# Kernel tuning notes

Measured on AMD Instinct MI355X. Metric: run time of the kernel, lower is better.

## Reference

```python
import jax, jax.numpy as jnp
import numpy as np

HEAD_DIM = 6
WS = 8  # window size
GROUPS = 4
EPS = 1e-5


def conv3x3(x, w, b):
    y = jax.lax.conv_general_dilated(x, w, (1, 1), [(1, 1), (1, 1)],
                                     dimension_numbers=('NCHW', 'OIHW', 'NCHW'))
    return y + b[None, :, None, None]


def conv1x1(x, w, b):
    # w: (O, C, 1, 1) pointwise conv == channel matmul
    return jnp.einsum('bchw,oc->bohw', x, w[:, :, 0, 0]) + b[None, :, None, None]


def group_norm(x, gamma, beta):
    B, C, H, W = x.shape
    xg = x.reshape(B, GROUPS, C // GROUPS, H, W)
    mu = xg.mean(axis=(2, 3, 4), keepdims=True)
    var = xg.var(axis=(2, 3, 4), keepdims=True)
    xg = (xg - mu) * jax.lax.rsqrt(var + EPS)
    return xg.reshape(B, C, H, W) * gamma[None, :, None, None] + beta[None, :, None, None]


def window_attention(x, qkv_w, qkv_b, proj_w, proj_b):
    # Per-window channel attention (attn is head_dim x head_dim, softmax over last dim).
    B, C, H, W = x.shape
    heads = C // HEAD_DIM
    scale = HEAD_DIM ** -0.5
    Hn, Wn = H // WS, W // WS
    L = WS * WS
    qkv = conv1x1(x, qkv_w, qkv_b)                       # (B, 3C, H, W); 1x1 conv commutes with windowing
    qkv = qkv.reshape(B, 3, heads, HEAD_DIM, Hn, WS, Wn, WS)
    qkv = qkv.transpose(1, 0, 4, 6, 2, 3, 5, 7).reshape(3, B, Hn, Wn, heads, HEAD_DIM, L)
    q, k, v = qkv[0], qkv[1], qkv[2]
    attn = jnp.einsum('bijhdl,bijhel->bijhde', q, k) * scale  # (B,Hn,Wn,heads,hd,hd)
    attn = jax.nn.softmax(attn, axis=-1)
    out = jnp.einsum('bijhde,bijhel->bijhdl', attn, v)
    out = out.reshape(B, Hn, Wn, heads, HEAD_DIM, WS, WS)
    out = out.transpose(0, 3, 4, 1, 5, 2, 6).reshape(B, C, H, W)
    return conv1x1(out, proj_w, proj_b)


def shifted_window_attention(x, qkv_w, qkv_b, proj_w, proj_b):
    B, C, H, W = x.shape
    pad_h = (WS - H % WS) % WS
    pad_w = (WS - W % WS) % WS
    if pad_h or pad_w:
        x = jnp.pad(x, ((0, 0), (0, 0), (0, pad_h), (0, pad_w)), mode='reflect')
    s = WS // 2
    x_sh = jnp.roll(x, shift=(-s, -s), axis=(2, 3))
    x1 = window_attention(x, qkv_w, qkv_b, proj_w, proj_b)
    x2 = window_attention(x_sh, qkv_w, qkv_b, proj_w, proj_b)
    x2 = jnp.roll(x2, shift=(s, s), axis=(2, 3))
    x = (x1 + x2) * 0.5
    return x[:, :, :H, :W]


def setup_inputs() -> dict:
    key = jax.random.key(0)
    ks = jax.random.split(key, 12)
    B, Cin, Cout, T, H, W = 16, 96, 96, 256, 128, 128
    std = 0.05
    return {
        'x': jax.random.normal(ks[0], (B, Cin, H, W), jnp.float32),
        't_emb': jax.random.normal(ks[1], (B, T), jnp.float32),
        'w1': jax.random.normal(ks[2], (Cout, Cin, 3, 3), jnp.float32) * std,
        'b1': jnp.zeros((Cout,), jnp.float32),
        'g1': jnp.ones((Cout,), jnp.float32),
        'be1': jnp.zeros((Cout,), jnp.float32),
        'wt': jax.random.normal(ks[3], (2 * Cout, T), jnp.float32) * std,
        'bt': jnp.zeros((2 * Cout,), jnp.float32),
        'qkv_w': jax.random.normal(ks[4], (3 * Cout, Cout, 1, 1), jnp.float32) * std,
        'qkv_b': jnp.zeros((3 * Cout,), jnp.float32),
        'proj_w': jax.random.normal(ks[5], (Cout, Cout, 1, 1), jnp.float32) * std,
        'proj_b': jnp.zeros((Cout,), jnp.float32),
        'ga': jnp.ones((Cout,), jnp.float32),
        'ba': jnp.zeros((Cout,), jnp.float32),
        'w2': jax.random.normal(ks[6], (Cout, Cout, 3, 3), jnp.float32) * std,
        'b2': jnp.zeros((Cout,), jnp.float32),
        'g2': jnp.ones((Cout,), jnp.float32),
        'be2': jnp.zeros((Cout,), jnp.float32),
    }


def reference(x, t_emb, w1, b1, g1, be1, wt, bt, qkv_w, qkv_b, proj_w, proj_b,
              ga, ba, w2, b2, g2, be2):
    C = w1.shape[0]
    # layer1: conv3x3 -> GN(4) -> SiLU
    h = jax.nn.silu(group_norm(conv3x3(x, w1, b1), g1, be1))
    # time FiLM
    t = jax.nn.silu(t_emb @ wt.T + bt)             # (B, 2C)
    shift, bias = t[:, :C], t[:, C:]
    h = h * (1.0 + shift[:, :, None, None]) + bias[:, :, None, None]
    residual = h
    h = group_norm(h, ga, ba)
    h = shifted_window_attention(h, qkv_w, qkv_b, proj_w, proj_b)
    h = residual + h
    # layer2: conv3x3 -> GN(4) -> SiLU
    h = jax.nn.silu(group_norm(conv3x3(h, w2, b2), g2, be2))
    return h
```

## Files before the change

kernel.cpp:

```cpp
#include <hip/hip_runtime.h>

#define B_   16
#define C_   96
#define H_   128
#define W_   128
#define HW_  16384
#define CPG_ 24
#define NPG_ 393216.0f
#define TDIM_ 256
#define PLANE_ ((size_t)B_ * C_ * HW_)

typedef unsigned short ushort_t;
typedef __bf16 bf16x8 __attribute__((ext_vector_type(8)));
typedef float  f32x4  __attribute__((ext_vector_type(4)));
typedef unsigned short u16x8 __attribute__((ext_vector_type(8)));
typedef unsigned short u16x4 __attribute__((ext_vector_type(4)));

#define ICP 104

__device__ __forceinline__ float silu_f(float x) { return x / (1.f + __expf(-x)); }
__device__ __forceinline__ float bf2f(ushort_t u) {
    union { float f; unsigned int i; } x; x.i = ((unsigned int)u) << 16; return x.f;
}
__device__ __forceinline__ ushort_t f2bf(float f) {
    __bf16 h = (__bf16)f; return *(ushort_t*)&h;
}

__global__ void temb_kernel(const float* __restrict__ t_emb,
                            const float* __restrict__ wt,
                            const float* __restrict__ bt,
                            float* __restrict__ tvec) {
    int idx = blockIdx.x * 256 + threadIdx.x;
    if (idx >= B_ * 192) return;
    int b = idx / 192, o = idx - b * 192;
    float a = bt[o];
    const float* te = t_emb + b * TDIM_;
    const float* wr = wt + o * TDIM_;
    for (int k = 0; k < TDIM_; ++k) a += te[k] * wr[k];
    tvec[idx] = silu_f(a);
}

__global__ void castbf_kernel(const float* __restrict__ src,
                              ushort_t* __restrict__ dst, int n4) {
    int i = blockIdx.x * 256 + threadIdx.x;
    if (i >= n4) return;
    float4 v = ((const float4*)src)[i];
    ushort4 u = { f2bf(v.x), f2bf(v.y), f2bf(v.z), f2bf(v.w) };
    ((ushort4*)dst)[i] = u;
}

__global__ void castw_kernel(const float* __restrict__ w1,
                             const float* __restrict__ w2,
                             ushort_t* __restrict__ wbf1,
                             ushort_t* __restrict__ wbf2) {
    int i = blockIdx.x * 256 + threadIdx.x;
    int ic = i % 96;
    int t  = i / 96;
    int oc = t % 96;
    int kk = t / 96;
    int src = (oc * 96 + ic) * 9 + kk;
    wbf1[i] = f2bf(w1[src]);
    wbf2[i] = f2bf(w2[src]);
}

__global__ __launch_bounds__(256, 2)
void conv3x3_mfma_kernel(const ushort_t* __restrict__ xbf,
                         const ushort_t* __restrict__ wbf,
                         const float* __restrict__ bias,
                         float* __restrict__ out,
                         float* __restrict__ stats) {
    __shared__ __align__(16) ushort_t ti[4 * 66 * ICP];
    __shared__ __align__(16) ushort_t wc[96 * ICP];
    __shared__ float red[4][96][2];

    const int b   = blockIdx.z;
    const int y0  = blockIdx.y * 2;
    const int x0  = blockIdx.x * 64;
    const int tid = threadIdx.x;
    const int wv   = tid >> 6;
    const int lane = tid & 63;
    const int l15  = lane & 15;
    const int quad = lane >> 4;

#pragma unroll
    for (int it = 0; it < 12; ++it) {
        int idx = it * 256 + tid;
        int ic = idx % 96;
        int t2 = idx / 96;
        int xc = t2 & 7;
        int r  = t2 >> 3;
        int gy = y0 - 1 + r;
        u16x8 v = {};
        if (gy >= 0 && gy < H_)
            v = *(const u16x8*)&xbf[((b * 96 + ic) * H_ + gy) * W_ + x0 + xc * 8];
        ushort_t* dst = &ti[(r * 66 + xc * 8 + 1) * ICP + ic];
#pragma unroll
        for (int j = 0; j < 8; ++j) dst[j * ICP] = v[j];
    }
    {
        int idx = tid;
#pragma unroll
        for (int it = 0; it < 3; ++it, idx += 256) {
            int ic = idx % 96;
            int t2 = idx / 96;
            int r = t2 >> 1, side = t2 & 1;
            int xi = side ? 65 : 0;
            int gx = x0 - 1 + xi;
            int gy = y0 - 1 + r;
            ushort_t vv = 0;
            if (gy >= 0 && gy < H_ && gx >= 0 && gx < W_)
                vv = xbf[((b * 96 + ic) * H_ + gy) * W_ + gx];
            ti[(r * 66 + xi) * ICP + ic] = vv;
        }
    }

    int wsrc[5], wdst[5];
#pragma unroll
    for (int i = 0; i < 5; ++i) {
        int idx = tid + i * 256;
        int icb = idx % 12;
        int oc  = idx / 12;
        wsrc[i] = oc * 96 + icb * 8;
        wdst[i] = oc * ICP + icb * 8;
    }
    u16x8 wreg[5];
#pragma unroll
    for (int i = 0; i < 4; ++i) wreg[i] = *(const u16x8*)&wbf[wsrc[i]];
    if (tid < 128) wreg[4] = *(const u16x8*)&wbf[wsrc[4]];

    f32x4 acc[2][6];
#pragma unroll
    for (int m = 0; m < 2; ++m)
#pragma unroll
        for (int nt = 0; nt < 6; ++nt)
            acc[m][nt] = (f32x4){0.f, 0.f, 0.f, 0.f};

    for (int kk = 0; kk < 9; ++kk) {
        const int ky = kk / 3, kx = kk - ky * 3;
        __syncthreads();
#pragma unroll
        for (int i = 0; i < 4; ++i) *(u16x8*)&wc[wdst[i]] = wreg[i];
        if (tid < 128) *(u16x8*)&wc[wdst[4]] = wreg[4];
        __syncthreads();
        if (kk < 8) {
            const ushort_t* wsk = wbf + (kk + 1) * 9216;
#pragma unroll
            for (int i = 0; i < 4; ++i) wreg[i] = *(const u16x8*)&wsk[wsrc[i]];
            if (tid < 128) wreg[4] = *(const u16x8*)&wsk[wsrc[4]];
        }
#pragma unroll 1
        for (int ck = 0; ck < 3; ++ck) {
            const int kbase = ck * 32 + quad * 8;
            bf16x8 a0 = *(const bf16x8*)&ti[((0 + ky) * 66 + (wv * 16 + l15 + kx)) * ICP + kbase];
            bf16x8 a1 = *(const bf16x8*)&ti[((1 + ky) * 66 + (wv * 16 + l15 + kx)) * ICP + kbase];
#pragma unroll
            for (int nt = 0; nt < 6; ++nt) {
                bf16x8 bv = *(const bf16x8*)&wc[(nt * 16 + l15) * ICP + kbase];
                acc[0][nt] = __builtin_amdgcn_mfma_f32_16x16x32_bf16(a0, bv, acc[0][nt], 0, 0, 0);
                acc[1][nt] = __builtin_amdgcn_mfma_f32_16x16x32_bf16(a1, bv, acc[1][nt], 0, 0, 0);
            }
        }
    }

    float lsum[6], lsq[6];
#pragma unroll
    for (int nt = 0; nt < 6; ++nt) { lsum[nt] = 0.f; lsq[nt] = 0.f; }

#pragma unroll
    for (int m = 0; m < 2; ++m) {
        const int gy = y0 + m;
        const int gx = x0 + wv * 16 + quad * 4;
#pragma unroll
        for (int nt = 0; nt < 6; ++nt) {
            const int oc = nt * 16 + l15;
            const float bz = bias[oc];
            float v0 = acc[m][nt][0] + bz;
            float v1 = acc[m][nt][1] + bz;
            float v2 = acc[m][nt][2] + bz;
            float v3 = acc[m][nt][3] + bz;
            float4 vv = make_float4(v0, v1, v2, v3);
            *(float4*)&out[((b * 96 + oc) * H_ + gy) * W_ + gx] = vv;
            lsum[nt] += v0 + v1 + v2 + v3;
            lsq[nt]  += v0 * v0 + v1 * v1 + v2 * v2 + v3 * v3;
        }
    }
#pragma unroll
    for (int nt = 0; nt < 6; ++nt) {
        float s = lsum[nt], q = lsq[nt];
        s += __shfl_down(s, 32, 64);
        s += __shfl_down(s, 16, 64);
        q += __shfl_down(q, 32, 64);
        q += __shfl_down(q, 16, 64);
        if (lane < 16) {
            red[wv][nt * 16 + lane][0] = s;
            red[wv][nt * 16 + lane][1] = q;
        }
    }
    __syncthreads();
    if (tid < 8) {
        const int g = tid >> 1, which = tid & 1;
        float v = 0.f;
        for (int oc = g * CPG_; oc < g * CPG_ + CPG_; ++oc)
            for (int w2 = 0; w2 < 4; ++w2) v += red[w2][oc][which];
        atomicAdd(&stats[(b * 4 + g) * 2 + which], v);
    }
}

__global__ void apply1_kernel(const float* y,
                              const float* __restrict__ stats1,
                              const float* __restrict__ g1,
                              const float* __restrict__ be1,
                              const float* __restrict__ tvec,
                              float* h,
                              float* __restrict__ stats2) {
    const int bc = blockIdx.x;
    const int b = bc / C_, c = bc - b * C_;
    const int g = c / CPG_;
    const float sum = stats1[(b * 4 + g) * 2], sumsq = stats1[(b * 4 + g) * 2 + 1];
    const float mean = sum / NPG_;
    const float var  = sumsq / NPG_ - mean * mean;
    const float rstd = rsqrtf(var + 1e-5f);
    const float sc = rstd * g1[c];
    const float sh = be1[c] - mean * sc;
    const float tsc = 1.f + tvec[b * 192 + c];
    const float tbi = tvec[b * 192 + 96 + c];

    const float4* yp = (const float4*)(y + (size_t)bc * HW_);
    float4* hp = (float4*)(h + (size_t)bc * HW_);
    float ls = 0.f, lss = 0.f;
    for (int i = threadIdx.x; i < HW_ / 4; i += 256) {
        float4 v = yp[i];
        float r0 = silu_f(v.x * sc + sh) * tsc + tbi;
        float r1 = silu_f(v.y * sc + sh) * tsc + tbi;
        float r2 = silu_f(v.z * sc + sh) * tsc + tbi;
        float r3 = silu_f(v.w * sc + sh) * tsc + tbi;
        hp[i] = make_float4(r0, r1, r2, r3);
        ls  += r0 + r1 + r2 + r3;
        lss += r0*r0 + r1*r1 + r2*r2 + r3*r3;
    }
    for (int off = 32; off > 0; off >>= 1) {
        ls  += __shfl_down(ls, off, 64);
        lss += __shfl_down(lss, off, 64);
    }
    if ((threadIdx.x & 63) == 0) {
        atomicAdd(&stats2[(b * 4 + g) * 2 + 0], ls);
        atomicAdd(&stats2[(b * 4 + g) * 2 + 1], lss);
    }
}

__global__ void gn_bf16_kernel(const float* __restrict__ in,
                               const float* __restrict__ stats,
                               const float* __restrict__ gamma,
                               const float* __restrict__ beta,
                               ushort_t* __restrict__ outb) {
    const int bc = blockIdx.x;
    const int b = bc / C_, c = bc - b * C_;
    const int g = c / CPG_;
    const float sum = stats[(b * 4 + g) * 2], sumsq = stats[(b * 4 + g) * 2 + 1];
    const float mean = sum / NPG_;
    const float var  = sumsq / NPG_ - mean * mean;
    const float rstd = rsqrtf(var + 1e-5f);
    const float sc = rstd * gamma[c];
    const float sh = beta[c] - mean * sc;
    const float4* ip = (const float4*)(in + (size_t)bc * HW_);
    ushort4* op = (ushort4*)(outb + (size_t)bc * HW_);
    for (int i = threadIdx.x; i < HW_ / 4; i += 256) {
        float4 v = ip[i];
        ushort4 u = { f2bf(v.x * sc + sh), f2bf(v.y * sc + sh),
                      f2bf(v.z * sc + sh), f2bf(v.w * sc + sh) };
        op[i] = u;
    }
}

__global__ void gn_apply_kernel(const float* in,
                                const float* __restrict__ stats,
                                const float* __restrict__ gamma,
                                const float* __restrict__ beta,
                                float* out, int dosilu) {
    const int bc = blockIdx.x;
    const int b = bc / C_, c = bc - b * C_;
    const int g = c / CPG_;
    const float sum = stats[(b * 4 + g) * 2], sumsq = stats[(b * 4 + g) * 2 + 1];
    const float mean = sum / NPG_;
    const float var  = sumsq / NPG_ - mean * mean;
    const float rstd = rsqrtf(var + 1e-5f);
    const float sc = rstd * gamma[c];
    const float sh = beta[c] - mean * sc;
    const float4* ip = (const float4*)(in + (size_t)bc * HW_);
    float4* op = (float4*)(out + (size_t)bc * HW_);
    for (int i = threadIdx.x; i < HW_ / 4; i += 256) {
        float4 v = ip[i];
        float r0 = v.x * sc + sh, r1 = v.y * sc + sh;
        float r2 = v.z * sc + sh, r3 = v.w * sc + sh;
        if (dosilu) { r0 = silu_f(r0); r1 = silu_f(r1); r2 = silu_f(r2); r3 = silu_f(r3); }
        op[i] = make_float4(r0, r1, r2, r3);
    }
}

__global__ __launch_bounds__(256, 3)
void qkv_gemm_kernel(const ushort_t* __restrict__ xq,
                     const float* __restrict__ qw,
                     const float* __restrict__ qb,
                     ushort_t* __restrict__ qkvbuf) {
    __shared__ __align__(16) ushort_t ti[2 * 64 * ICP];
    __shared__ __align__(16) ushort_t wc[96 * ICP];

    const int bz = blockIdx.z;
    const int b = bz / 3, s = bz - b * 3;
    const int y0 = blockIdx.y * 2;
    const int x0 = blockIdx.x * 64;
    const int tid = threadIdx.x;
    const int wv = tid >> 6, lane = tid & 63;
    const int l15 = lane & 15, quad = lane >> 4;

#pragma unroll
    for (int it = 0; it < 6; ++it) {
        int idx = it * 256 + tid;
        int ic = idx % 96;
        int t2 = idx / 96;
        int xc = t2 & 7;
        int r  = t2 >> 3;
        u16x8 v = *(const u16x8*)&xq[((b * 96 + ic) * H_ + y0 + r) * W_ + x0 + xc * 8];
        ushort_t* dst = &ti[(r * 64 + xc * 8) * ICP + ic];
#pragma unroll
        for (int j = 0; j < 8; ++j) dst[j * ICP] = v[j];
    }
#pragma unroll
    for (int it = 0; it < 9; ++it) {
        int idx = it * 256 + tid;
        int icq = idx % 24;
        int oc  = idx / 24;
        float4 wv4 = *(const float4*)&qw[(s * 96 + oc) * 96 + icq * 4];
        ushort4 u = { f2bf(wv4.x), f2bf(wv4.y), f2bf(wv4.z), f2bf(wv4.w) };
        *(ushort4*)&wc[oc * ICP + icq * 4] = u;
    }
    __syncthreads();

    f32x4 acc[2][6];
#pragma unroll
    for (int m = 0; m < 2; ++m)
#pragma unroll
        for (int nt = 0; nt < 6; ++nt) acc[m][nt] = (f32x4){0.f, 0.f, 0.f, 0.f};

#pragma unroll
    for (int ck = 0; ck < 3; ++ck) {
        const int kbase = ck * 32 + quad * 8;
        bf16x8 a0 = *(const bf16x8*)&ti[(0 * 64 + wv * 16 + l15) * ICP + kbase];
        bf16x8 a1 = *(const bf16x8*)&ti[(1 * 64 + wv * 16 + l15) * ICP + kbase];
#pragma unroll
        for (int nt = 0; nt < 6; ++nt) {
            bf16x8 bv = *(const bf16x8*)&wc[(nt * 16 + l15) * ICP + kbase];
            acc[0][nt] = __builtin_amdgcn_mfma_f32_16x16x32_bf16(a0, bv, acc[0][nt], 0, 0, 0);
            acc[1][nt] = __builtin_amdgcn_mfma_f32_16x16x32_bf16(a1, bv, acc[1][nt], 0, 0, 0);
        }
    }

#pragma unroll
    for (int m = 0; m < 2; ++m) {
        const int gy = y0 + m;
        const int gx = x0 + wv * 16 + quad * 4;
#pragma unroll
        for (int nt = 0; nt < 6; ++nt) {
            const int ocg = s * 96 + nt * 16 + l15;
            const float bz2 = qb[ocg];
            ushort4 u = { f2bf(acc[m][nt][0] + bz2), f2bf(acc[m][nt][1] + bz2),
                          f2bf(acc[m][nt][2] + bz2), f2bf(acc[m][nt][3] + bz2) };
            *(ushort4*)&qkvbuf[((size_t)(b * 288 + ocg) * H_ + gy) * W_ + gx] = u;
        }
    }
}

#define QKC 1288
#define QKR 160
#define OSTS 1032
#define VTS 520
__global__ __launch_bounds__(256, 2)
void attn2_kernel(const ushort_t* __restrict__ qkv,
                  ushort_t* __restrict__ obuf, int shift, int accumulate) {
    __shared__ __align__(16) ushort_t qk[12 * QKC];
    __shared__ __align__(16) ushort_t vt[16 * VTS + 32];
    __shared__ __align__(16) ushort_t ost[6 * OSTS];

    const int h = blockIdx.x, wy = blockIdx.y, b = blockIdx.z;
    const int tid = threadIdx.x;
    const int wv = tid >> 6, lane = tid & 63;
    const int l15 = lane & 15, quad = lane >> 4;

    for (int idx = tid; idx < 2304; idx += 256) {
        int xc = idx & 15;
        int t2 = idx >> 4;
        int r  = t2 & 7;
        int ch = t2 >> 3;
        int part = ch / 6, d = ch - part * 6;
        int gch = part * 96 + h * 6 + d;
        int gy = (wy * 8 + r + shift) & 127;
        size_t rowb = ((size_t)(b * 288 + gch) * H_ + gy) * W_;
        ushort4 u0, u1;
        if (shift == 0) {
            u0 = *(const ushort4*)&qkv[rowb + xc * 8];
            u1 = *(const ushort4*)&qkv[rowb + xc * 8 + 4];
        } else {
            u0 = *(const ushort4*)&qkv[rowb + ((xc * 8 + 4) & 127)];
            u1 = *(const ushort4*)&qkv[rowb + ((xc * 8 + 8) & 127)];
        }
        ushort_t* dst = (part < 2) ? &qk[ch * QKC + r * QKR + xc * 8]
                                   : &ost[d * OSTS + r * 128 + xc * 8];
        *(ushort4*)dst = u0;
        *(ushort4*)(dst + 4) = u1;
    }
    __syncthreads();

    {
        const int r   = tid >> 5;
        const int pxq = tid & 31;
        const int px  = pxq * 4;
        u16x4 vv[6];
#pragma unroll
        for (int c = 0; c < 6; ++c)
            vv[c] = *(const u16x4*)&ost[c * OSTS + r * 128 + px];
        const int wx = px >> 3;
        const int p7 = px & 7;
#pragma unroll
        for (int j = 0; j < 4; ++j) {
            u16x8 t;
            t[0] = vv[0][j]; t[1] = vv[1][j]; t[2] = vv[2][j];
            t[3] = vv[3][j]; t[4] = vv[4][j]; t[5] = vv[5][j];
            t[6] = 0; t[7] = 0;
            *(u16x8*)&vt[wx * VTS + (r * 8 + p7 + j) * 8] = t;
        }
        if (tid < 16) ((unsigned int*)(vt + 16 * VTS))[tid] = 0u;
    }
    __syncthreads();

    const float scale = 0.40824829046386302f;
    const int dcl = (l15 < 6) ? l15 : 5;
    const int chA = 6 + dcl;
    const int chB = dcl;

    for (int i = 0; i < 4; ++i) {
        const int wx = wv * 4 + i;
        f32x4 sa = (f32x4){0.f, 0.f, 0.f, 0.f};
#pragma unroll
        for (int ck = 0; ck < 2; ++ck) {
            const int r = ck * 4 + quad;
            bf16x8 af  = *(const bf16x8*)&qk[chA * QKC + r * QKR + wx * 8];
            bf16x8 bfv = *(const bf16x8*)&qk[chB * QKC + r * QKR + wx * 8];
            sa = __builtin_amdgcn_mfma_f32_16x16x32_bf16(af, bfv, sa, 0, 0, 0);
        }
        float s0 = sa[0] * scale, s1 = sa[1] * scale, s2 = sa[2] * scale, s3 = sa[3] * scale;
        float m = -3.4e38f;
        if (quad == 0) m = fmaxf(fmaxf(s0, s1), fmaxf(s2, s3));
        else if (quad == 1) m = fmaxf(s0, s1);
        m = fmaxf(m, __shfl_xor(m, 16, 64));
        m = fmaxf(m, __shfl_xor(m, 32, 64));
        float p0 = (quad <= 1) ? __expf(s0 - m) : 0.f;
        float p1 = (quad <= 1) ? __expf(s1 - m) : 0.f;
        float p2 = (quad == 0) ? __expf(s2 - m) : 0.f;
        float p3 = (quad == 0) ? __expf(s3 - m) : 0.f;
        float sum = p0 + p1 + p2 + p3;
        sum += __shfl_xor(sum, 16, 64);
        sum += __shfl_xor(sum, 32, 64);
        float inv = 1.f / sum;
        p0 *= inv; p1 *= inv; p2 *= inv; p3 *= inv;
        float e4 = __shfl_xor(p0, 16, 64);
        float e5 = __shfl_xor(p1, 16, 64);
        bf16x8 pf;
        pf[0] = (__bf16)p0; pf[1] = (__bf16)p1; pf[2] = (__bf16)p2; pf[3] = (__bf16)p3;
        pf[4] = (__bf16)e4; pf[5] = (__bf16)e5;
        pf[6] = (__bf16)0.f; pf[7] = (__bf16)0.f;
        if (quad != 0) { bf16x8 z = {}; pf = z; }
#pragma unroll
        for (int mt = 0; mt < 4; ++mt) {
            bf16x8 av = *(const bf16x8*)&vt[wx * VTS + (mt * 16 + l15) * 8 + quad * 8];
            f32x4 o = __builtin_amdgcn_mfma_f32_16x16x32_bf16(av, pf, (f32x4){0.f,0.f,0.f,0.f}, 0, 0, 0);
            if (l15 < 6) {
                const int px = mt * 16 + quad * 4;
                const int r = px >> 3, c = px & 7;
                ushort4 st = { f2bf(o[0]), f2bf(o[1]), f2bf(o[2]), f2bf(o[3]) };
                *(ushort4*)&ost[l15 * OSTS + r * 128 + wx * 8 + c] = st;
            }
        }
    }
    __syncthreads();

    for (int idx = tid; idx < 768; idx += 256) {
        int xc = idx & 15;
        int t2 = idx >> 4;
        int r = t2 & 7, d = t2 >> 3;
        int gy = (wy * 8 + r + shift) & 127;
        size_t rowb = ((size_t)(b * 96 + h * 6 + d) * H_ + gy) * W_;
        size_t a0, a1;
        if (shift == 0) { a0 = rowb + xc * 8; a1 = rowb + xc * 8 + 4; }
        else { a0 = rowb + ((xc * 8 + 4) & 127); a1 = rowb + ((xc * 8 + 8) & 127); }
        const ushort_t* src = &ost[d * OSTS + r * 128 + xc * 8];
        ushort4 v0 = *(const ushort4*)src;
        ushort4 v1 = *(const ushort4*)(src + 4);
        if (accumulate) {
            ushort4 q0 = *(const ushort4*)&obuf[a0];
            ushort4 q1 = *(const ushort4*)&obuf[a1];
            v0.x = f2bf(0.5f * (bf2f(v0.x) + bf2f(q0.x)));
            v0.y = f2bf(0.5f * (bf2f(v0.y) + bf2f(q0.y)));
            v0.z = f2bf(0.5f * (bf2f(v0.z) + bf2f(q0.z)));
            v0.w = f2bf(0.5f * (bf2f(v0.w) + bf2f(q0.w)));
            v1.x = f2bf(0.5f * (bf2f(v1.x) + bf2f(q1.x)));
            v1.y = f2bf(0.5f * (bf2f(v1.y) + bf2f(q1.y)));
            v1.z = f2bf(0.5f * (bf2f(v1.z) + bf2f(q1.z)));
            v1.w = f2bf(0.5f * (bf2f(v1.w) + bf2f(q1.w)));
        }
        *(ushort4*)&obuf[a0] = v0;
        *(ushort4*)&obuf[a1] = v1;
    }
}

__global__ __launch_bounds__(256, 3)
void proj_gemm_kernel(const ushort_t* __restrict__ ob,
                      const float* __restrict__ pw,
                      const float* __restrict__ pb,
                      const float* __restrict__ resid,
                      ushort_t* __restrict__ h2) {
    __shared__ __align__(16) ushort_t ti[2 * 64 * ICP];
    __shared__ __align__(16) ushort_t wc[96 * ICP];

    const int b = blockIdx.z;
    const int y0 = blockIdx.y * 2;
    const int x0 = blockIdx.x * 64;
    const int tid = threadIdx.x;
    const int wv = tid >> 6, lane = tid & 63;
    const int l15 = lane & 15, quad = lane >> 4;

#pragma unroll
    for (int it = 0; it < 6; ++it) {
        int idx = it * 256 + tid;
        int ic = idx % 96;
        int t2 = idx / 96;
        int xc = t2 & 7;
        int r  = t2 >> 3;
        u16x8 v = *(const u16x8*)&ob[((b * 96 + ic) * H_ + y0 + r) * W_ + x0 + xc * 8];
        ushort_t* dst = &ti[(r * 64 + xc * 8) * ICP + ic];
#pragma unroll
        for (int j = 0; j < 8; ++j) dst[j * ICP] = v[j];
    }
#pragma unroll
    for (int it = 0; it < 9; ++it) {
        int idx = it * 256 + tid;
        int icq = idx % 24;
        int oc  = idx / 24;
        float4 wv4 = *(const float4*)&pw[oc * 96 + icq * 4];
        ushort4 u = { f2bf(wv4.x), f2bf(wv4.y), f2bf(wv4.z), f2bf(wv4.w) };
        *(ushort4*)&wc[oc * ICP + icq * 4] = u;
    }
    __syncthreads();

    f32x4 acc[2][6];
#pragma unroll
    for (int m = 0; m < 2; ++m)
#pragma unroll
        for (int nt = 0; nt < 6; ++nt) acc[m][nt] = (f32x4){0.f, 0.f, 0.f, 0.f};

#pragma unroll
    for (int ck = 0; ck < 3; ++ck) {
        const int kbase = ck * 32 + quad * 8;
        bf16x8 a0 = *(const bf16x8*)&ti[(0 * 64 + wv * 16 + l15) * ICP + kbase];
        bf16x8 a1 = *(const bf16x8*)&ti[(1 * 64 + wv * 16 + l15) * ICP + kbase];
#pragma unroll
        for (int nt = 0; nt < 6; ++nt) {
            bf16x8 bv = *(const bf16x8*)&wc[(nt * 16 + l15) * ICP + kbase];
            acc[0][nt] = __builtin_amdgcn_mfma_f32_16x16x32_bf16(a0, bv, acc[0][nt], 0, 0, 0);
            acc[1][nt] = __builtin_amdgcn_mfma_f32_16x16x32_bf16(a1, bv, acc[1][nt], 0, 0, 0);
        }
    }

#pragma unroll
    for (int m = 0; m < 2; ++m) {
        const int gy = y0 + m;
        const int gx = x0 + wv * 16 + quad * 4;
#pragma unroll
        for (int nt = 0; nt < 6; ++nt) {
            const int oc = nt * 16 + l15;
            const float bz2 = pb[oc];
            size_t addr = ((size_t)(b * 96 + oc) * H_ + gy) * W_ + gx;
            float4 rv = *(const float4*)&resid[addr];
            ushort4 u = { f2bf(acc[m][nt][0] + bz2 + rv.x),
                          f2bf(acc[m][nt][1] + bz2 + rv.y),
                          f2bf(acc[m][nt][2] + bz2 + rv.z),
                          f2bf(acc[m][nt][3] + bz2 + rv.w) };
            *(ushort4*)&h2[addr] = u;
        }
    }
}

extern "C" void kernel_launch(void* const* d_in, const int* in_sizes, int n_in,
                              void* d_out, int out_size, void* d_ws, size_t ws_size,
                              hipStream_t stream) {
    const float* x     = (const float*)d_in[0];
    const float* t_emb = (const float*)d_in[1];
    const float* w1    = (const float*)d_in[2];
    const float* b1    = (const float*)d_in[3];
    const float* g1    = (const float*)d_in[4];
    const float* be1   = (const float*)d_in[5];
    const float* wt    = (const float*)d_in[6];
    const float* bt    = (const float*)d_in[7];
    const float* qkv_w = (const float*)d_in[8];
    const float* qkv_b = (const float*)d_in[9];
    const float* proj_w= (const float*)d_in[10];
    const float* proj_b= (const float*)d_in[11];
    const float* ga    = (const float*)d_in[12];
    const float* ba    = (const float*)d_in[13];
    const float* w2    = (const float*)d_in[14];
    const float* b2    = (const float*)d_in[15];
    const float* g2    = (const float*)d_in[16];
    const float* be2   = (const float*)d_in[17];

    float* out = (float*)d_out;

    ushort_t* A  = (ushort_t*)d_ws;
    ushort_t* Bq = A + PLANE_;
    float* stats = (float*)(Bq + 3 * PLANE_);
    float* tvec  = stats + 384;
    ushort_t* wbf1 = (ushort_t*)(tvec + 3072);
    ushort_t* wbf2 = wbf1 + 82944;

    hipMemsetAsync(stats, 0, 384 * sizeof(float), stream);
    temb_kernel<<<12, 256, 0, stream>>>(t_emb, wt, bt, tvec);
    castw_kernel<<<324, 256, 0, stream>>>(w1, w2, wbf1, wbf2);

    castbf_kernel<<<(int)(PLANE_ / 4 / 256), 256, 0, stream>>>(x, A, (int)(PLANE_ / 4));
    conv3x3_mfma_kernel<<<dim3(2, 64, 16), 256, 0, stream>>>(A, wbf1, b1, out, stats);

    apply1_kernel<<<B_ * C_, 256, 0, stream>>>(out, stats, g1, be1, tvec, out, stats + 128);
    gn_bf16_kernel<<<B_ * C_, 256, 0, stream>>>(out, stats + 128, ga, ba, A);

    qkv_gemm_kernel<<<dim3(2, 64, 48), 256, 0, stream>>>(A, qkv_w, qkv_b, Bq);

    attn2_kernel<<<dim3(16, 16, 16), 256, 0, stream>>>(Bq, A, 0, 0);
    attn2_kernel<<<dim3(16, 16, 16), 256, 0, stream>>>(Bq, A, 4, 1);

    proj_gemm_kernel<<<dim3(2, 64, 16), 256, 0, stream>>>(A, proj_w, proj_b, out, Bq);

    conv3x3_mfma_kernel<<<dim3(2, 64, 16), 256, 0, stream>>>(Bq, wbf2, b2, out, stats + 256);

    gn_apply_kernel<<<B_ * C_, 256, 0, stream>>>(out, stats + 256, g2, be2, out, 1);
}
```

Before: 781.9 us.

## Fuse input bf16 cast into conv3x3 and stream rows through two-slot LDS

Removes the separate fp32-to-bf16 cast kernel by templating the conv3x3 kernel to read fp32 input directly and convert it while staging into LDS. The input tile now holds two rows, refilled at kernel rows 3 and 6, instead of four, which halves that LDS buffer; launch bounds rise to 3 blocks per SM for more occupancy. This saves one full-plane write and read pass, but adds staging work inside the main loop behind the existing barrier and reads fp32 input at twice the bytes.

```diff
diff --git a/kernel.cpp b/kernel.cpp
--- a/kernel.cpp
+++ b/kernel.cpp
@@ -40,15 +40,6 @@
     tvec[idx] = silu_f(a);
 }
 
-__global__ void castbf_kernel(const float* __restrict__ src,
-                              ushort_t* __restrict__ dst, int n4) {
-    int i = blockIdx.x * 256 + threadIdx.x;
-    if (i >= n4) return;
-    float4 v = ((const float4*)src)[i];
-    ushort4 u = { f2bf(v.x), f2bf(v.y), f2bf(v.z), f2bf(v.w) };
-    ((ushort4*)dst)[i] = u;
-}
-
 __global__ void castw_kernel(const float* __restrict__ w1,
                              const float* __restrict__ w2,
                              ushort_t* __restrict__ wbf1,
@@ -63,13 +54,55 @@
     wbf2[i] = f2bf(w2[src]);
 }
 
-__global__ __launch_bounds__(256, 2)
-void conv3x3_mfma_kernel(const ushort_t* __restrict__ xbf,
+template<int FP32>
+__device__ __forceinline__ void stage_row(const void* __restrict__ xin,
+                                          ushort_t* __restrict__ ti2,
+                                          int b, int gy, int x0, int slot, int tid) {
+    const bool rowok = (gy >= 0 && gy < H_);
+#pragma unroll
+    for (int it = 0; it < 3; ++it) {
+        int idx = it * 256 + tid;
+        int ic = idx % 96;
+        int xc = idx / 96;
+        u16x8 v = {};
+        if (rowok) {
+            if (FP32) {
+                const float* xf = (const float*)xin;
+                const float4* p = (const float4*)&xf[((size_t)(b * 96 + ic) * H_ + gy) * W_ + x0 + xc * 8];
+                float4 f0 = p[0], f1 = p[1];
+                v[0] = f2bf(f0.x); v[1] = f2bf(f0.y); v[2] = f2bf(f0.z); v[3] = f2bf(f0.w);
+                v[4] = f2bf(f1.x); v[5] = f2bf(f1.y); v[6] = f2bf(f1.z); v[7] = f2bf(f1.w);
+            } else {
+                const ushort_t* xb = (const ushort_t*)xin;
+                v = *(const u16x8*)&xb[((size_t)(b * 96 + ic) * H_ + gy) * W_ + x0 + xc * 8];
+            }
+        }
+        ushort_t* dst = &ti2[(slot * 66 + xc * 8 + 1) * ICP + ic];
+#pragma unroll
+        for (int j = 0; j < 8; ++j) dst[j * ICP] = v[j];
+    }
+    if (tid < 192) {
+        int ic = tid % 96;
+        int side = tid / 96;
+        int xi = side ? 65 : 0;
+        int gx = x0 - 1 + xi;
+        ushort_t vv = 0;
+        if (rowok && gx >= 0 && gx < W_) {
+            if (FP32) vv = f2bf(((const float*)xin)[((size_t)(b * 96 + ic) * H_ + gy) * W_ + gx]);
+            else      vv = ((const ushort_t*)xin)[((size_t)(b * 96 + ic) * H_ + gy) * W_ + gx];
+        }
+        ti2[(slot * 66 + xi) * ICP + ic] = vv;
+    }
+}
+
+template<int FP32>
+__global__ __launch_bounds__(256, 3)
+void conv3x3_mfma_kernel(const void* __restrict__ xin,
                          const ushort_t* __restrict__ wbf,
                          const float* __restrict__ bias,
                          float* __restrict__ out,
                          float* __restrict__ stats) {
-    __shared__ __align__(16) ushort_t ti[4 * 66 * ICP];
+    __shared__ __align__(16) ushort_t ti2[2 * 66 * ICP];
     __shared__ __align__(16) ushort_t wc[96 * ICP];
     __shared__ float red[4][96][2];
 
@@ -82,37 +115,8 @@
     const int l15  = lane & 15;
     const int quad = lane >> 4;
 
-#pragma unroll
-    for (int it = 0; it < 12; ++it) {
-        int idx = it * 256 + tid;
-        int ic = idx % 96;
-        int t2 = idx / 96;
-        int xc = t2 & 7;
-        int r  = t2 >> 3;
-        int gy = y0 - 1 + r;
-        u16x8 v = {};
-        if (gy >= 0 && gy < H_)
-            v = *(const u16x8*)&xbf[((b * 96 + ic) * H_ + gy) * W_ + x0 + xc * 8];
-        ushort_t* dst = &ti[(r * 66 + xc * 8 + 1) * ICP + ic];
-#pragma unroll
-        for (int j = 0; j < 8; ++j) dst[j * ICP] = v[j];
-    }
-    {
-        int idx = tid;
-#pragma unroll
-        for (int it = 0; it < 3; ++it, idx += 256) {
-            int ic = idx % 96;
-            int t2 = idx / 96;
-            int r = t2 >> 1, side = t2 & 1;
-            int xi = side ? 65 : 0;
-            int gx = x0 - 1 + xi;
-            int gy = y0 - 1 + r;
-            ushort_t vv = 0;
-            if (gy >= 0 && gy < H_ && gx >= 0 && gx < W_)
-                vv = xbf[((b * 96 + ic) * H_ + gy) * W_ + gx];
-            ti[(r * 66 + xi) * ICP + ic] = vv;
-        }
-    }
+    stage_row<FP32>(xin, ti2, b, y0 - 1, x0, 0, tid);
+    stage_row<FP32>(xin, ti2, b, y0 + 0, x0, 1, tid);
 
     int wsrc[5], wdst[5];
 #pragma unroll
@@ -135,12 +139,19 @@
         for (int nt = 0; nt < 6; ++nt)
             acc[m][nt] = (f32x4){0.f, 0.f, 0.f, 0.f};
 
+#pragma unroll 1
     for (int kk = 0; kk < 9; ++kk) {
-        const int ky = kk / 3, kx = kk - ky * 3;
+        const int ky = (kk >= 6) ? 2 : (kk >= 3 ? 1 : 0);
+        const int kx = kk - 3 * ky;
+        const int sA = ky & 1;
+        const int sB = sA ^ 1;
+
         __syncthreads();
 #pragma unroll
         for (int i = 0; i < 4; ++i) *(u16x8*)&wc[wdst[i]] = wreg[i];
         if (tid < 128) *(u16x8*)&wc[wdst[4]] = wreg[4];
+        if (kk == 3)      stage_row<FP32>(xin, ti2, b, y0 + 1, x0, 0, tid);
+        else if (kk == 6) stage_row<FP32>(xin, ti2, b, y0 + 2, x0, 1, tid);
         __syncthreads();
         if (kk < 8) {
             const ushort_t* wsk = wbf + (kk + 1) * 9216;
@@ -151,8 +162,8 @@
 #pragma unroll 1
         for (int ck = 0; ck < 3; ++ck) {
             const int kbase = ck * 32 + quad * 8;
-            bf16x8 a0 = *(const bf16x8*)&ti[((0 + ky) * 66 + (wv * 16 + l15 + kx)) * ICP + kbase];
-            bf16x8 a1 = *(const bf16x8*)&ti[((1 + ky) * 66 + (wv * 16 + l15 + kx)) * ICP + kbase];
+            bf16x8 a0 = *(const bf16x8*)&ti2[(sA * 66 + (wv * 16 + l15 + kx)) * ICP + kbase];
+            bf16x8 a1 = *(const bf16x8*)&ti2[(sB * 66 + (wv * 16 + l15 + kx)) * ICP + kbase];
 #pragma unroll
             for (int nt = 0; nt < 6; ++nt) {
                 bf16x8 bv = *(const bf16x8*)&wc[(nt * 16 + l15) * ICP + kbase];
@@ -179,7 +190,7 @@
             float v2 = acc[m][nt][2] + bz;
             float v3 = acc[m][nt][3] + bz;
             float4 vv = make_float4(v0, v1, v2, v3);
-            *(float4*)&out[((b * 96 + oc) * H_ + gy) * W_ + gx] = vv;
+            *(float4*)&out[((size_t)(b * 96 + oc) * H_ + gy) * W_ + gx] = vv;
             lsum[nt] += v0 + v1 + v2 + v3;
             lsq[nt]  += v0 * v0 + v1 * v1 + v2 * v2 + v3 * v3;
         }
@@ -320,7 +331,7 @@
         int t2 = idx / 96;
         int xc = t2 & 7;
         int r  = t2 >> 3;
-        u16x8 v = *(const u16x8*)&xq[((b * 96 + ic) * H_ + y0 + r) * W_ + x0 + xc * 8];
+        u16x8 v = *(const u16x8*)&xq[((size_t)(b * 96 + ic) * H_ + y0 + r) * W_ + x0 + xc * 8];
         ushort_t* dst = &ti[(r * 64 + xc * 8) * ICP + ic];
 #pragma unroll
         for (int j = 0; j < 8; ++j) dst[j * ICP] = v[j];
@@ -535,7 +546,7 @@
         int t2 = idx / 96;
         int xc = t2 & 7;
         int r  = t2 >> 3;
-        u16x8 v = *(const u16x8*)&ob[((b * 96 + ic) * H_ + y0 + r) * W_ + x0 + xc * 8];
+        u16x8 v = *(const u16x8*)&ob[((size_t)(b * 96 + ic) * H_ + y0 + r) * W_ + x0 + xc * 8];
         ushort_t* dst = &ti[(r * 64 + xc * 8) * ICP + ic];
 #pragma unroll
         for (int j = 0; j < 8; ++j) dst[j * ICP] = v[j];
@@ -624,8 +635,7 @@
     temb_kernel<<<12, 256, 0, stream>>>(t_emb, wt, bt, tvec);
     castw_kernel<<<324, 256, 0, stream>>>(w1, w2, wbf1, wbf2);
 
-    castbf_kernel<<<(int)(PLANE_ / 4 / 256), 256, 0, stream>>>(x, A, (int)(PLANE_ / 4));
-    conv3x3_mfma_kernel<<<dim3(2, 64, 16), 256, 0, stream>>>(A, wbf1, b1, out, stats);
+    conv3x3_mfma_kernel<1><<<dim3(2, 64, 16), 256, 0, stream>>>((const void*)x, wbf1, b1, out, stats);
 
     apply1_kernel<<<B_ * C_, 256, 0, stream>>>(out, stats, g1, be1, tvec, out, stats + 128);
     gn_bf16_kernel<<<B_ * C_, 256, 0, stream>>>(out, stats + 128, ga, ba, A);
@@ -637,7 +647,7 @@
 
     proj_gemm_kernel<<<dim3(2, 64, 16), 256, 0, stream>>>(A, proj_w, proj_b, out, Bq);
 
-    conv3x3_mfma_kernel<<<dim3(2, 64, 16), 256, 0, stream>>>(Bq, wbf2, b2, out, stats + 256);
+    conv3x3_mfma_kernel<0><<<dim3(2, 64, 16), 256, 0, stream>>>((const void*)Bq, wbf2, b2, out, stats + 256);
 
     gn_apply_kernel<<<B_ * C_, 256, 0, stream>>>(out, stats + 256, g2, be2, out, 1);
 }
```

Measured after the change: 727.1 us. 7.0% less time.
